# Kernel optimization log

Hardware: AMD Instinct MI355X
Metric: run time of the kernel (lower is better)

Reference implementation:

```python
import math
import jax, jax.numpy as jnp
import numpy as np

B, T, C, H = 2, 2048, 1024, 16
HD = C // H
ALPHA = 32.0


def setup_inputs() -> dict:
    key = jax.random.key(0)
    ks = jax.random.split(key, 16)
    s = 0.02
    inp = {
        "query": jax.random.normal(ks[0], (B, T, C), jnp.float32),
        "key": jax.random.normal(ks[1], (B, T, C), jnp.float32),
        "value": jax.random.normal(ks[2], (B, T, C), jnp.float32),
        # causal mask: 0 => masked (matches masked_fill(att_mask == 0, -inf))
        "att_mask": jnp.tril(jnp.ones((1, 1, T, T), jnp.float32)),
        "Wq": jax.random.normal(ks[3], (C, C), jnp.float32) * s,
        "bq": jnp.zeros((C,), jnp.float32),
        "Wk": jax.random.normal(ks[4], (C, C), jnp.float32) * s,
        "bk": jnp.zeros((C,), jnp.float32),
        "Wv": jax.random.normal(ks[5], (C, C), jnp.float32) * s,
        "bv": jnp.zeros((C,), jnp.float32),
        "Wp": jax.random.normal(ks[6], (C, C), jnp.float32) * s,
        "bp": jnp.zeros((C,), jnp.float32),
    }
    return inp


def reference(query, key, value, att_mask, Wq, bq, Wk, bk, Wv, bv, Wp, bp):
    b, tq, c = query.shape
    tk = key.shape[1]
    # separate QKV projections, split heads: [B,H,T,HD]
    q = (query @ Wq + bq).reshape(b, tq, H, HD).transpose(0, 2, 1, 3)
    k = (key @ Wk + bk).reshape(b, tk, H, HD).transpose(0, 2, 1, 3)
    v = (value @ Wv + bv).reshape(b, tk, H, HD).transpose(0, 2, 1, 3)
    # PBrelax: pre-scale q by 1/(alpha*sqrt(hd)), subtract detached global abs-max, rescale
    att = jnp.einsum("bhqd,bhkd->bhqk", q * (1.0 / ALPHA / math.sqrt(HD)), k)
    att = (att - jax.lax.stop_gradient(jnp.max(jnp.abs(att)))) * ALPHA
    att = jnp.where(att_mask[:, :, :tq, :tk] == 0, -jnp.inf, att)
    att = jax.nn.softmax(att, axis=-1)
    y = jnp.einsum("bhqk,bhkd->bhqd", att, v)
    y = y.transpose(0, 2, 1, 3).reshape(b, tq, c)
    return y @ Wp + bp
```

## Files before the change

### kernel.cpp

```cpp
#include <hip/hip_runtime.h>


#define Bsz 2
#define Tsz 2048
#define Csz 1024
#define Hsz 16
#define HDsz 64

typedef __bf16 bf16;
typedef __bf16 bf16x8 __attribute__((ext_vector_type(8)));
typedef __bf16 bf16x4 __attribute__((ext_vector_type(4)));
typedef float float4v __attribute__((ext_vector_type(4)));

#define MFMA16(a, b, c) __builtin_amdgcn_mfma_f32_16x16x32_bf16(a, b, c, 0, 0, 0)

#define GLOAD_LDS16(gptr, lptr)                                      \
  __builtin_amdgcn_global_load_lds(                                  \
      (const __attribute__((address_space(1))) void*)(gptr),         \
      (__attribute__((address_space(3))) void*)(lptr), 16, 0, 0)

__global__ __launch_bounds__(256) void prep_bf16(
    const float* __restrict__ q, const float* __restrict__ k,
    const float* __restrict__ v, bf16* __restrict__ oq,
    bf16* __restrict__ ok, bf16* __restrict__ ov,
    const float* __restrict__ Wq, const float* __restrict__ Wk,
    const float* __restrict__ Wv, const float* __restrict__ Wp,
    bf16* __restrict__ WT) {
  __shared__ float Ts[64][68];
  const int bid = (int)blockIdx.x;
  const int tid = threadIdx.x;
  if (bid < 6144) {
    const int z = bid >> 11;
    const int xb = bid & 2047;
    const float* src = z == 0 ? q : (z == 1 ? k : v);
    bf16* dst = z == 0 ? oq : (z == 1 ? ok : ov);
    const size_t i = ((size_t)xb * 256 + tid) * 8;
    const float4 a = *(const float4*)(src + i);
    const float4 b = *(const float4*)(src + i + 4);
    bf16x8 o;
    o[0] = (bf16)a.x; o[1] = (bf16)a.y; o[2] = (bf16)a.z; o[3] = (bf16)a.w;
    o[4] = (bf16)b.x; o[5] = (bf16)b.y; o[6] = (bf16)b.z; o[7] = (bf16)b.w;
    *(bf16x8*)(dst + i) = o;
  } else {
    const int w = bid - 6144;
    const int z = w >> 8;
    const int rem = w & 255;
    const int k0 = (rem >> 4) * 64, n0 = (rem & 15) * 64;
    const float* W = z == 0 ? Wq : (z == 1 ? Wk : (z == 2 ? Wv : Wp));
    bf16* out = WT + (size_t)z * (Csz * Csz);
#pragma unroll
    for (int it = 0; it < 4; ++it) {
      const int idx = it * 256 + tid;
      const int r = idx >> 4, c4 = (idx & 15) * 4;
      *(float4*)&Ts[r][c4] =
          *(const float4*)(W + (size_t)(k0 + r) * Csz + n0 + c4);
    }
    __syncthreads();
#pragma unroll
    for (int it = 0; it < 2; ++it) {
      const int idx = it * 256 + tid;
      const int n = idx & 63, k8 = (idx >> 6) * 8;
      bf16x8 o;
#pragma unroll
      for (int j = 0; j < 8; ++j) o[j] = (bf16)Ts[k8 + j][n];
      *(bf16x8*)(out + (size_t)(n0 + n) * Csz + k0 + k8) = o;
    }
  }
}

__global__ __launch_bounds__(512, 2) void gemm256_qkv(
    const bf16* __restrict__ A0, const bf16* __restrict__ A1,
    const bf16* __restrict__ A2, const bf16* __restrict__ Wt,
    const float* __restrict__ b0, const float* __restrict__ b1,
    const float* __restrict__ b2, bf16* __restrict__ C0,
    bf16* __restrict__ C1, bf16* __restrict__ Vt) {
  constexpr int NT = Csz / 64;
  const int z = blockIdx.z;
  const bf16* A = z == 0 ? A0 : (z == 1 ? A1 : A2);
  const float* bias = z == 0 ? b0 : (z == 1 ? b1 : b2);
  const bf16* Bt = Wt + (size_t)z * (Csz * Csz);
  const int m0 = blockIdx.y * 256;
  const int nz0 = blockIdx.x * 256;

  __shared__ bf16 As[2 * 256 * 64];
  __shared__ bf16 Bs[2 * 256 * 64];

  const int tid = threadIdx.x;
  const int wave = tid >> 6, lane = tid & 63;
  const int l15 = lane & 15, quad = lane >> 4;
  const int wm = wave >> 2, wn = wave & 3;

  const int srow = tid >> 3;
  const int sch = tid & 7;
  const bf16* Ab = A + (size_t)(m0 + srow) * Csz + (sch ^ (srow & 7)) * 8;
  const bf16* Bb = Bt + (size_t)(nz0 + srow) * Csz + (sch ^ (srow & 7)) * 8;

#define STG(Xb, lds, lbuf, hh, tt)                                           \
  {                                                                          \
    GLOAD_LDS16((Xb) + (size_t)((hh)*128) * Csz + (size_t)(tt)*64,           \
                &(lds)[(lbuf) * (256 * 64) + (hh)*8192 + tid * 8]);          \
    GLOAD_LDS16((Xb) + (size_t)((hh)*128 + 64) * Csz + (size_t)(tt)*64,     \
                &(lds)[(lbuf) * (256 * 64) + (hh)*8192 + 4096 + tid * 8]);  \
  }
#define RD_A(dst, lbuf, i2, ks)                                              \
  dst = *(const bf16x8*)&As[(lbuf) * (256 * 64) +                            \
                            (wm * 128 + (i2)*16 + l15) * 64 +                \
                            ((((ks)*4 + quad) ^ (l15 & 7)) * 8)];
#define RD_B(dst, lbuf, j2, ks)                                              \
  dst = *(const bf16x8*)&Bs[(lbuf) * (256 * 64) +                            \
                            (wn * 64 + (j2)*16 + l15) * 64 +                 \
                            ((((ks)*4 + quad) ^ (l15 & 7)) * 8)];

  float4v acc[8][4];
#pragma unroll
  for (int i = 0; i < 8; ++i)
#pragma unroll
    for (int j = 0; j < 4; ++j) acc[i][j] = (float4v){0.f, 0.f, 0.f, 0.f};

  STG(Ab, As, 0, 0, 0);
  STG(Ab, As, 0, 1, 0);
  STG(Bb, Bs, 0, 0, 0);
  STG(Bb, Bs, 0, 1, 0);
  STG(Ab, As, 1, 0, 1);
  STG(Ab, As, 1, 1, 1);
  asm volatile("s_waitcnt vmcnt(4)" ::: "memory");
  __builtin_amdgcn_s_barrier();
  __builtin_amdgcn_sched_barrier(0);

#pragma unroll 1
  for (int t = 0; t < NT; ++t) {
    const int bsel = t & 1;
    bf16x8 af0[4][2], af1[4][2], bf0[2][2], bf1[2][2];

#pragma unroll
    for (int i = 0; i < 4; ++i) {
      RD_A(af0[i][0], bsel, i, 0);
      RD_A(af0[i][1], bsel, i, 1);
    }
#pragma unroll
    for (int j = 0; j < 2; ++j) {
      RD_B(bf0[j][0], bsel, j, 0);
      RD_B(bf0[j][1], bsel, j, 1);
    }
    if (t + 1 < NT) STG(Bb, Bs, bsel ^ 1, 0, t + 1);
    __builtin_amdgcn_s_barrier();
    asm volatile("s_waitcnt lgkmcnt(0)" ::: "memory");
    __builtin_amdgcn_sched_barrier(0);
    __builtin_amdgcn_s_setprio(1);
#pragma unroll
    for (int i = 0; i < 4; ++i)
#pragma unroll
      for (int j = 0; j < 2; ++j) {
        acc[i][j] = MFMA16(af0[i][0], bf0[j][0], acc[i][j]);
        acc[i][j] = MFMA16(af0[i][1], bf0[j][1], acc[i][j]);
      }
    __builtin_amdgcn_s_setprio(0);
    __builtin_amdgcn_s_barrier();

#pragma unroll
    for (int i = 0; i < 4; ++i) {
      RD_A(af1[i][0], bsel, 4 + i, 0);
      RD_A(af1[i][1], bsel, 4 + i, 1);
    }
    if (t + 1 < NT) STG(Bb, Bs, bsel ^ 1, 1, t + 1);
    __builtin_amdgcn_s_barrier();
    asm volatile("s_waitcnt lgkmcnt(0)" ::: "memory");
    __builtin_amdgcn_sched_barrier(0);
    __builtin_amdgcn_s_setprio(1);
#pragma unroll
    for (int i = 0; i < 4; ++i)
#pragma unroll
      for (int j = 0; j < 2; ++j) {
        acc[4 + i][j] = MFMA16(af1[i][0], bf0[j][0], acc[4 + i][j]);
        acc[4 + i][j] = MFMA16(af1[i][1], bf0[j][1], acc[4 + i][j]);
      }
    __builtin_amdgcn_s_setprio(0);
    __builtin_amdgcn_s_barrier();

#pragma unroll
    for (int j = 0; j < 2; ++j) {
      RD_B(bf1[j][0], bsel, 2 + j, 0);
      RD_B(bf1[j][1], bsel, 2 + j, 1);
    }
    if (t + 2 < NT) STG(Ab, As, bsel, 0, t + 2);
    __builtin_amdgcn_s_barrier();
    asm volatile("s_waitcnt lgkmcnt(0)" ::: "memory");
    __builtin_amdgcn_sched_barrier(0);
    __builtin_amdgcn_s_setprio(1);
#pragma unroll
    for (int i = 0; i < 4; ++i)
#pragma unroll
      for (int j = 0; j < 2; ++j) {
        acc[i][2 + j] = MFMA16(af0[i][0], bf1[j][0], acc[i][2 + j]);
        acc[i][2 + j] = MFMA16(af0[i][1], bf1[j][1], acc[i][2 + j]);
      }
    __builtin_amdgcn_s_setprio(0);
    __builtin_amdgcn_s_barrier();

    if (t + 2 < NT) STG(Ab, As, bsel, 1, t + 2);
    __builtin_amdgcn_s_barrier();
    __builtin_amdgcn_s_setprio(1);
#pragma unroll
    for (int i = 0; i < 4; ++i)
#pragma unroll
      for (int j = 0; j < 2; ++j) {
        acc[4 + i][2 + j] = MFMA16(af1[i][0], bf1[j][0], acc[4 + i][2 + j]);
        acc[4 + i][2 + j] = MFMA16(af1[i][1], bf1[j][1], acc[4 + i][2 + j]);
      }
    __builtin_amdgcn_s_setprio(0);
    if (t + 2 < NT) {
      asm volatile("s_waitcnt vmcnt(4)" ::: "memory");
    } else if (t + 1 < NT) {
      asm volatile("s_waitcnt vmcnt(0)" ::: "memory");
    }
    __builtin_amdgcn_s_barrier();
    __builtin_amdgcn_sched_barrier(0);
  }
#undef STG
#undef RD_A
#undef RD_B

  const int omb0 = m0 + wm * 128 + quad * 4;
  const int onb0 = nz0 + wn * 64 + l15;
  if (z == 2) {
#pragma unroll
    for (int j = 0; j < 4; ++j) {
      const int n = onb0 + j * 16;
      const float bj = bias[n];
#pragma unroll
      for (int i = 0; i < 8; ++i) {
        const int mrow = omb0 + i * 16;
        const int bb = mrow >> 11, tt = mrow & (Tsz - 1);
        union { bf16 h[4]; uint2 u; } pk;
#pragma unroll
        for (int r = 0; r < 4; ++r) pk.h[r] = (bf16)(acc[i][j][r] + bj);
        *(uint2*)(Vt + ((size_t)(bb * 1024 + n)) * Tsz + tt) = pk.u;
      }
    }
  } else {
    bf16* C = z == 0 ? C0 : C1;
    const float osc = z == 0 ? 0.180336880111124f : 1.0f;
#pragma unroll
    for (int j = 0; j < 4; ++j) {
      const float bj = bias[onb0 + j * 16];
#pragma unroll
      for (int i = 0; i < 8; ++i) {
#pragma unroll
        for (int r = 0; r < 4; ++r) {
          const float v = (acc[i][j][r] + bj) * osc;
          C[(size_t)(omb0 + i * 16 + r) * Csz + onb0 + j * 16] = (bf16)v;
        }
      }
    }
  }
}

__global__ __launch_bounds__(256) void gemm_op(
    const bf16* __restrict__ A, const bf16* __restrict__ Bt,
    const float* __restrict__ bias, float* __restrict__ C) {
  __shared__ bf16 As[128 * 32];
  __shared__ bf16 Bs[64 * 32];
  const int tid = threadIdx.x;
  const int wave = tid >> 6, lane = tid & 63;
  const int l15 = lane & 15, quad = lane >> 4;
  const int m0 = blockIdx.y * 128, n0 = blockIdx.x * 64;
  const int wm = (wave >> 1) * 64, wn = (wave & 1) * 32;
  const int srow = tid >> 2, schunk = tid & 3;

  float4v acc[4][2];
#pragma unroll
  for (int i = 0; i < 4; ++i)
#pragma unroll
    for (int j = 0; j < 2; ++j) acc[i][j] = (float4v){0.f, 0.f, 0.f, 0.f};

  for (int k0 = 0; k0 < Csz; k0 += 32) {
    __syncthreads();
#pragma unroll
    for (int p = 0; p < 2; ++p) {
      const int row = p * 64 + srow;
      GLOAD_LDS16(A + (size_t)(m0 + row) * Csz + k0 + schunk * 8,
                  &As[(p * 256 + tid) * 8]);
    }
    GLOAD_LDS16(Bt + (size_t)(n0 + srow) * Csz + k0 + schunk * 8,
                &Bs[tid * 8]);
    __syncthreads();

    bf16x8 af[4], bfr[2];
#pragma unroll
    for (int i = 0; i < 4; ++i)
      af[i] = *(const bf16x8*)&As[(wm + i * 16 + l15) * 32 + quad * 8];
#pragma unroll
    for (int j = 0; j < 2; ++j)
      bfr[j] = *(const bf16x8*)&Bs[(wn + j * 16 + l15) * 32 + quad * 8];
#pragma unroll
    for (int i = 0; i < 4; ++i)
#pragma unroll
      for (int j = 0; j < 2; ++j)
        acc[i][j] = MFMA16(af[i], bfr[j], acc[i][j]);
  }

  const int omb = m0 + wm + quad * 4;
  const int onb = n0 + wn + l15;
#pragma unroll
  for (int j = 0; j < 2; ++j) {
    const float bj = bias[onb + j * 16];
#pragma unroll
    for (int i = 0; i < 4; ++i) {
#pragma unroll
      for (int r = 0; r < 4; ++r)
        C[(size_t)(omb + i * 16 + r) * Csz + onb + j * 16] =
            acc[i][j][r] + bj;
    }
  }
}

__global__ __launch_bounds__(256) void attn_mfma(const bf16* __restrict__ Q,
                                                 const bf16* __restrict__ K,
                                                 const bf16* __restrict__ Vt,
                                                 bf16* __restrict__ Y) {
  __shared__ bf16 Ks[2][64 * 64];
  __shared__ bf16 Vs[2][64 * 64];
  __shared__ bf16 Ps[4][32 * 72];

  const int bh = blockIdx.y;
  const int b = bh >> 4, h = bh & 15;
  const int xr = (int)(gridDim.x - 1 - blockIdx.x);
  const int i0 = xr * 128;
  const int tid = threadIdx.x;
  const int wave = tid >> 6, lane = tid & 63;
  const int l15 = lane & 15, quad = lane >> 4;

  const int srow = tid >> 3;
  const int sch = tid & 7;

  const bf16* kb = K + (size_t)b * Tsz * Csz + h * HDsz;
  const bf16* vb = Vt + (size_t)bh * HDsz * Tsz;

  const int qb = i0 + wave * 32;

  bf16x8 qf[2][2];
#pragma unroll
  for (int sub = 0; sub < 2; ++sub) {
    const bf16* qp =
        Q + ((size_t)(b * Tsz + qb + sub * 16 + l15)) * Csz + h * HDsz + quad * 8;
    qf[sub][0] = *(const bf16x8*)qp;
    qf[sub][1] = *(const bf16x8*)(qp + 32);
  }

  bf16x8 ones;
#pragma unroll
  for (int j = 0; j < 8; ++j) ones[j] = (bf16)1.0f;

  float4v Of[2][4];
  float4v accl[2];
#pragma unroll
  for (int sub = 0; sub < 2; ++sub) {
    accl[sub] = (float4v){0.f, 0.f, 0.f, 0.f};
#pragma unroll
    for (int nc = 0; nc < 4; ++nc) Of[sub][nc] = (float4v){0.f, 0.f, 0.f, 0.f};
  }

  const int ntile = i0 / 64 + 2;
  const int s0 = ((int)blockIdx.x ^ bh ^ (bh >> 4)) & 1;

#define STAGE_KV(tt, bb)                                                     \
  {                                                                          \
    _Pragma("unroll") for (int p = 0; p < 2; ++p) {                          \
      const int r = p * 32 + srow;                                           \
      const int c = sch ^ (r & 7);                                           \
      GLOAD_LDS16(kb + (size_t)((tt)*64 + r) * Csz + c * 8,                  \
                  &Ks[bb][(p * 256 + tid) * 8]);                             \
      GLOAD_LDS16(vb + (size_t)r * Tsz + (tt)*64 + c * 8,                    \
                  &Vs[bb][(p * 256 + tid) * 8]);                             \
    }                                                                        \
  }

  STAGE_KV(s0, 0);
  asm volatile("s_waitcnt vmcnt(0)" ::: "memory");
  __builtin_amdgcn_s_barrier();
  __builtin_amdgcn_sched_barrier(0);

#pragma unroll 1
  for (int s = 0; s < ntile; ++s) {
    int tp = s + s0;
    if (tp >= ntile) tp -= ntile;
    const int j0 = tp * 64;
    const int buf = s & 1;
    if (s + 1 < ntile) {
      int tn = tp + 1;
      if (tn >= ntile) tn -= ntile;
      STAGE_KV(tn, buf ^ 1);
    }

    if (j0 <= qb + 31) {
      float4v S[2][4];
#pragma unroll
      for (int nc = 0; nc < 4; ++nc) {
        const int row = nc * 16 + l15;
        const bf16x8 k0 =
            *(const bf16x8*)&Ks[buf][row * 64 + ((quad ^ (row & 7)) * 8)];
        const bf16x8 k1 =
            *(const bf16x8*)&Ks[buf][row * 64 + (((quad + 4) ^ (row & 7)) * 8)];
#pragma unroll
        for (int sub = 0; sub < 2; ++sub) {
          float4v a = (float4v){0.f, 0.f, 0.f, 0.f};
          a = MFMA16(k0, qf[sub][0], a);
          a = MFMA16(k1, qf[sub][1], a);
          S[sub][nc] = a;
        }
      }

      if (j0 + 63 > qb) {
#pragma unroll
        for (int sub = 0; sub < 2; ++sub) {
          const int q = qb + sub * 16 + l15;
#pragma unroll
          for (int nc = 0; nc < 4; ++nc) {
            const int keyb = j0 + nc * 16 + quad * 4;
#pragma unroll
            for (int r = 0; r < 4; ++r)
              if (keyb + r > q) S[sub][nc][r] = -1e30f;
          }
        }
      }

#pragma unroll
      for (int sub = 0; sub < 2; ++sub) {
#pragma unroll
        for (int nc = 0; nc < 4; ++nc) {
          bf16x4 pk;
#pragma unroll
          for (int r = 0; r < 4; ++r)
            pk[r] = (bf16)__builtin_amdgcn_exp2f(S[sub][nc][r]);
          *(bf16x4*)&Ps[wave][(sub * 16 + l15) * 72 + nc * 16 + quad * 4] = pk;
        }
      }

      bf16x8 pf[2][2];
#pragma unroll
      for (int sub = 0; sub < 2; ++sub) {
#pragma unroll
        for (int kc = 0; kc < 2; ++kc)
          pf[sub][kc] = *(const bf16x8*)
              &Ps[wave][(sub * 16 + l15) * 72 + kc * 32 + quad * 8];
        accl[sub] = MFMA16(ones, pf[sub][0], accl[sub]);
        accl[sub] = MFMA16(ones, pf[sub][1], accl[sub]);
      }
#pragma unroll
      for (int nc = 0; nc < 4; ++nc) {
        const int row = nc * 16 + l15;
#pragma unroll
        for (int kc = 0; kc < 2; ++kc) {
          const bf16x8 vf = *(const bf16x8*)
              &Vs[buf][row * 64 + (((kc * 4 + quad) ^ (row & 7)) * 8)];
#pragma unroll
          for (int sub = 0; sub < 2; ++sub)
            Of[sub][nc] = MFMA16(vf, pf[sub][kc], Of[sub][nc]);
        }
      }
    }

    if (s + 1 < ntile) {
      asm volatile("s_waitcnt vmcnt(0)" ::: "memory");
    }
    __builtin_amdgcn_sched_barrier(0);
    __builtin_amdgcn_s_barrier();
    __builtin_amdgcn_sched_barrier(0);
  }
#undef STAGE_KV

#pragma unroll
  for (int sub = 0; sub < 2; ++sub) {
    const float rl = __builtin_amdgcn_rcpf(accl[sub][0]);
    const size_t rowoff =
        ((size_t)(b * Tsz + qb + sub * 16 + l15)) * Csz + h * HDsz;
#pragma unroll
    for (int nc = 0; nc < 4; ++nc) {
      union { bf16 h4[4]; uint2 u; } pk;
#pragma unroll
      for (int r = 0; r < 4; ++r) pk.h4[r] = (bf16)(Of[sub][nc][r] * rl);
      *(uint2*)(Y + rowoff + nc * 16 + quad * 4) = pk.u;
    }
  }
}

extern "C" void kernel_launch(void* const* d_in, const int* in_sizes, int n_in,
                              void* d_out, int out_size, void* d_ws,
                              size_t ws_size, hipStream_t stream) {
  const float* query = (const float*)d_in[0];
  const float* key = (const float*)d_in[1];
  const float* value = (const float*)d_in[2];
  const float* Wq = (const float*)d_in[4];
  const float* bq = (const float*)d_in[5];
  const float* Wk = (const float*)d_in[6];
  const float* bk = (const float*)d_in[7];
  const float* Wv = (const float*)d_in[8];
  const float* bv = (const float*)d_in[9];
  const float* Wp = (const float*)d_in[10];
  const float* bp = (const float*)d_in[11];
  float* out = (float*)d_out;

  char* ws = (char*)d_ws;
  bf16* WT = (bf16*)(ws);
  bf16* vc = (bf16*)(ws + (8u << 20));
  bf16* Qp = (bf16*)(ws + (16u << 20));
  bf16* Kp = (bf16*)(ws + (24u << 20));
  bf16* Vt = (bf16*)(ws + (32u << 20));
  bf16* Yb = vc;
  bf16* qc = (bf16*)d_out;
  bf16* kc = (bf16*)((char*)d_out + (8u << 20));

  const int M = Bsz * Tsz;

  prep_bf16<<<dim3(7168), dim3(256), 0, stream>>>(query, key, value, qc, kc,
                                                  vc, Wq, Wk, Wv, Wp, WT);
  gemm256_qkv<<<dim3(Csz / 256, M / 256, 3), dim3(512), 0, stream>>>(
      qc, kc, vc, WT, bq, bk, bv, Qp, Kp, Vt);
  attn_mfma<<<dim3(Tsz / 128, Bsz * Hsz), dim3(256), 0, stream>>>(Qp, Kp, Vt,
                                                                  Yb);
  gemm_op<<<dim3(Csz / 64, M / 128), dim3(256), 0, stream>>>(
      Yb, WT + 3u * (Csz * Csz), bp, out);
}
```

Baseline: 251.1 us.

## Split attention block into 8 waves of 16 query rows with interleaved tile order

The attention kernel now launches 512 threads per block, with each of eight waves handling 16 query rows instead of four waves handling 32. Each thread stages one K/V chunk per tile instead of two, and the rotated tile start offset is dropped. Block-to-query-tile mapping now alternates short and long causal rows and is mirrored for the second batch, to balance work across CUs. The aim is more waves to hide latency and fewer registers per wave, at the cost of each K/V LDS fragment being reused by only one 16-row MFMA group instead of two.

Result: faster. 226.7 us (-9.7%).

```diff
diff --git a/kernel.cpp b/kernel.cpp
--- a/kernel.cpp
+++ b/kernel.cpp
@@ -314,17 +314,19 @@
   }
 }
 
-__global__ __launch_bounds__(256) void attn_mfma(const bf16* __restrict__ Q,
+__global__ __launch_bounds__(512) void attn_mfma(const bf16* __restrict__ Q,
                                                  const bf16* __restrict__ K,
                                                  const bf16* __restrict__ Vt,
                                                  bf16* __restrict__ Y) {
   __shared__ bf16 Ks[2][64 * 64];
   __shared__ bf16 Vs[2][64 * 64];
-  __shared__ bf16 Ps[4][32 * 72];
+  __shared__ bf16 Ps[8][16 * 72];
 
   const int bh = blockIdx.y;
   const int b = bh >> 4, h = bh & 15;
-  const int xr = (int)(gridDim.x - 1 - blockIdx.x);
+  int xr = (blockIdx.x & 1) ? (int)(gridDim.x - 1 - (blockIdx.x >> 1))
+                            : (int)(blockIdx.x >> 1);
+  if (bh >= 16) xr = (int)(gridDim.x - 1) - xr;
   const int i0 = xr * 128;
   const int tid = threadIdx.x;
   const int wave = tid >> 6, lane = tid & 63;
@@ -336,64 +338,49 @@
   const bf16* kb = K + (size_t)b * Tsz * Csz + h * HDsz;
   const bf16* vb = Vt + (size_t)bh * HDsz * Tsz;
 
-  const int qb = i0 + wave * 32;
-
-  bf16x8 qf[2][2];
-#pragma unroll
-  for (int sub = 0; sub < 2; ++sub) {
+  const int qb = i0 + wave * 16;
+
+  bf16x8 qf[2];
+  {
     const bf16* qp =
-        Q + ((size_t)(b * Tsz + qb + sub * 16 + l15)) * Csz + h * HDsz + quad * 8;
-    qf[sub][0] = *(const bf16x8*)qp;
-    qf[sub][1] = *(const bf16x8*)(qp + 32);
+        Q + ((size_t)(b * Tsz + qb + l15)) * Csz + h * HDsz + quad * 8;
+    qf[0] = *(const bf16x8*)qp;
+    qf[1] = *(const bf16x8*)(qp + 32);
   }
 
   bf16x8 ones;
 #pragma unroll
   for (int j = 0; j < 8; ++j) ones[j] = (bf16)1.0f;
 
-  float4v Of[2][4];
-  float4v accl[2];
-#pragma unroll
-  for (int sub = 0; sub < 2; ++sub) {
-    accl[sub] = (float4v){0.f, 0.f, 0.f, 0.f};
-#pragma unroll
-    for (int nc = 0; nc < 4; ++nc) Of[sub][nc] = (float4v){0.f, 0.f, 0.f, 0.f};
-  }
+  float4v Of[4];
+  float4v accl = (float4v){0.f, 0.f, 0.f, 0.f};
+#pragma unroll
+  for (int nc = 0; nc < 4; ++nc) Of[nc] = (float4v){0.f, 0.f, 0.f, 0.f};
 
   const int ntile = i0 / 64 + 2;
-  const int s0 = ((int)blockIdx.x ^ bh ^ (bh >> 4)) & 1;
 
 #define STAGE_KV(tt, bb)                                                     \
   {                                                                          \
-    _Pragma("unroll") for (int p = 0; p < 2; ++p) {                          \
-      const int r = p * 32 + srow;                                           \
-      const int c = sch ^ (r & 7);                                           \
-      GLOAD_LDS16(kb + (size_t)((tt)*64 + r) * Csz + c * 8,                  \
-                  &Ks[bb][(p * 256 + tid) * 8]);                             \
-      GLOAD_LDS16(vb + (size_t)r * Tsz + (tt)*64 + c * 8,                    \
-                  &Vs[bb][(p * 256 + tid) * 8]);                             \
-    }                                                                        \
-  }
-
-  STAGE_KV(s0, 0);
+    const int c = sch ^ (srow & 7);                                          \
+    GLOAD_LDS16(kb + (size_t)((tt)*64 + srow) * Csz + c * 8,                 \
+                &Ks[bb][tid * 8]);                                           \
+    GLOAD_LDS16(vb + (size_t)srow * Tsz + (tt)*64 + c * 8,                   \
+                &Vs[bb][tid * 8]);                                           \
+  }
+
+  STAGE_KV(0, 0);
   asm volatile("s_waitcnt vmcnt(0)" ::: "memory");
   __builtin_amdgcn_s_barrier();
   __builtin_amdgcn_sched_barrier(0);
 
 #pragma unroll 1
-  for (int s = 0; s < ntile; ++s) {
-    int tp = s + s0;
-    if (tp >= ntile) tp -= ntile;
-    const int j0 = tp * 64;
-    const int buf = s & 1;
-    if (s + 1 < ntile) {
-      int tn = tp + 1;
-      if (tn >= ntile) tn -= ntile;
-      STAGE_KV(tn, buf ^ 1);
-    }
-
-    if (j0 <= qb + 31) {
-      float4v S[2][4];
+  for (int t = 0; t < ntile; ++t) {
+    const int j0 = t * 64;
+    const int buf = t & 1;
+    if (t + 1 < ntile) STAGE_KV(t + 1, buf ^ 1);
+
+    if (j0 <= qb + 15) {
+      float4v S[4];
 #pragma unroll
       for (int nc = 0; nc < 4; ++nc) {
         const int row = nc * 16 + l15;
@@ -401,51 +388,38 @@
             *(const bf16x8*)&Ks[buf][row * 64 + ((quad ^ (row & 7)) * 8)];
         const bf16x8 k1 =
             *(const bf16x8*)&Ks[buf][row * 64 + (((quad + 4) ^ (row & 7)) * 8)];
-#pragma unroll
-        for (int sub = 0; sub < 2; ++sub) {
-          float4v a = (float4v){0.f, 0.f, 0.f, 0.f};
-          a = MFMA16(k0, qf[sub][0], a);
-          a = MFMA16(k1, qf[sub][1], a);
-          S[sub][nc] = a;
+        float4v a = (float4v){0.f, 0.f, 0.f, 0.f};
+        a = MFMA16(k0, qf[0], a);
+        a = MFMA16(k1, qf[1], a);
+        S[nc] = a;
+      }
+
+      if (j0 + 63 > qb) {
+        const int q = qb + l15;
+#pragma unroll
+        for (int nc = 0; nc < 4; ++nc) {
+          const int keyb = j0 + nc * 16 + quad * 4;
+#pragma unroll
+          for (int r = 0; r < 4; ++r)
+            if (keyb + r > q) S[nc][r] = -1e30f;
         }
       }
 
-      if (j0 + 63 > qb) {
-#pragma unroll
-        for (int sub = 0; sub < 2; ++sub) {
-          const int q = qb + sub * 16 + l15;
-#pragma unroll
-          for (int nc = 0; nc < 4; ++nc) {
-            const int keyb = j0 + nc * 16 + quad * 4;
-#pragma unroll
-            for (int r = 0; r < 4; ++r)
-              if (keyb + r > q) S[sub][nc][r] = -1e30f;
-          }
-        }
-      }
-
-#pragma unroll
-      for (int sub = 0; sub < 2; ++sub) {
-#pragma unroll
-        for (int nc = 0; nc < 4; ++nc) {
-          bf16x4 pk;
-#pragma unroll
-          for (int r = 0; r < 4; ++r)
-            pk[r] = (bf16)__builtin_amdgcn_exp2f(S[sub][nc][r]);
-          *(bf16x4*)&Ps[wave][(sub * 16 + l15) * 72 + nc * 16 + quad * 4] = pk;
-        }
-      }
-
-      bf16x8 pf[2][2];
-#pragma unroll
-      for (int sub = 0; sub < 2; ++sub) {
-#pragma unroll
-        for (int kc = 0; kc < 2; ++kc)
-          pf[sub][kc] = *(const bf16x8*)
-              &Ps[wave][(sub * 16 + l15) * 72 + kc * 32 + quad * 8];
-        accl[sub] = MFMA16(ones, pf[sub][0], accl[sub]);
-        accl[sub] = MFMA16(ones, pf[sub][1], accl[sub]);
-      }
+#pragma unroll
+      for (int nc = 0; nc < 4; ++nc) {
+        bf16x4 pk;
+#pragma unroll
+        for (int r = 0; r < 4; ++r)
+          pk[r] = (bf16)__builtin_amdgcn_exp2f(S[nc][r]);
+        *(bf16x4*)&Ps[wave][l15 * 72 + nc * 16 + quad * 4] = pk;
+      }
+
+      bf16x8 pf[2];
+#pragma unroll
+      for (int kc = 0; kc < 2; ++kc)
+        pf[kc] = *(const bf16x8*)&Ps[wave][l15 * 72 + kc * 32 + quad * 8];
+      accl = MFMA16(ones, pf[0], accl);
+      accl = MFMA16(ones, pf[1], accl);
 #pragma unroll
       for (int nc = 0; nc < 4; ++nc) {
         const int row = nc * 16 + l15;
@@ -453,14 +427,12 @@
         for (int kc = 0; kc < 2; ++kc) {
           const bf16x8 vf = *(const bf16x8*)
               &Vs[buf][row * 64 + (((kc * 4 + quad) ^ (row & 7)) * 8)];
-#pragma unroll
-          for (int sub = 0; sub < 2; ++sub)
-            Of[sub][nc] = MFMA16(vf, pf[sub][kc], Of[sub][nc]);
+          Of[nc] = MFMA16(vf, pf[kc], Of[nc]);
         }
       }
     }
 
-    if (s + 1 < ntile) {
+    if (t + 1 < ntile) {
       asm volatile("s_waitcnt vmcnt(0)" ::: "memory");
     }
     __builtin_amdgcn_sched_barrier(0);
@@ -469,16 +441,14 @@
   }
 #undef STAGE_KV
 
-#pragma unroll
-  for (int sub = 0; sub < 2; ++sub) {
-    const float rl = __builtin_amdgcn_rcpf(accl[sub][0]);
-    const size_t rowoff =
-        ((size_t)(b * Tsz + qb + sub * 16 + l15)) * Csz + h * HDsz;
+  {
+    const float rl = __builtin_amdgcn_rcpf(accl[0]);
+    const size_t rowoff = ((size_t)(b * Tsz + qb + l15)) * Csz + h * HDsz;
 #pragma unroll
     for (int nc = 0; nc < 4; ++nc) {
       union { bf16 h4[4]; uint2 u; } pk;
 #pragma unroll
-      for (int r = 0; r < 4; ++r) pk.h4[r] = (bf16)(Of[sub][nc][r] * rl);
+      for (int r = 0; r < 4; ++r) pk.h4[r] = (bf16)(Of[nc][r] * rl);
       *(uint2*)(Y + rowoff + nc * 16 + quad * 4) = pk.u;
     }
   }
@@ -516,7 +486,7 @@
                                                   vc, Wq, Wk, Wv, Wp, WT);
   gemm256_qkv<<<dim3(Csz / 256, M / 256, 3), dim3(512), 0, stream>>>(
       qc, kc, vc, WT, bq, bk, bv, Qp, Kp, Vt);
-  attn_mfma<<<dim3(Tsz / 128, Bsz * Hsz), dim3(256), 0, stream>>>(Qp, Kp, Vt,
+  attn_mfma<<<dim3(Tsz / 128, Bsz * Hsz), dim3(512), 0, stream>>>(Qp, Kp, Vt,
                                                                   Yb);
   gemm_op<<<dim3(Csz / 64, M / 128), dim3(256), 0, stream>>>(
       Yb, WT + 3u * (Csz * Csz), bp, out);
```
